# Kernel tuning notes

Hardware: AMD Instinct MI355X
Metric: run time of the kernel (lower is better)

Reference implementation:

```python
import jax, jax.numpy as jnp
import numpy as np

D = 128  # head dim

def setup_inputs() -> dict:
    key = jax.random.key(0)
    k1, k2, k3, k4, k5 = jax.random.split(key, 5)
    B, N, M, C1, C2 = 4, 4096, 4096, 1024, 1024
    x = jax.random.normal(k1, (B, N, C1), dtype=jnp.float32)
    y = jax.random.normal(k2, (B, M, C2), dtype=jnp.float32)
    # Linear(c, d, bias=False): out = inp @ W where W is [c, d]
    Wq = jax.random.normal(k3, (C1, D), dtype=jnp.float32) / np.sqrt(C1)
    Wk = jax.random.normal(k4, (C2, D), dtype=jnp.float32) / np.sqrt(C2)
    Wv = jax.random.normal(k5, (C2, D), dtype=jnp.float32) / np.sqrt(C2)
    return {"x": x, "y": y, "Wq": Wq, "Wk": Wk, "Wv": Wv}

def reference(x, y, Wq, Wk, Wv):
    q = x @ Wq                               # [B, N, d]
    k = y @ Wk                               # [B, M, d]
    v = y @ Wv                               # [B, M, d]
    scale = 1.0 / jnp.sqrt(jnp.asarray(D, dtype=q.dtype))
    a = jnp.einsum('bnd,bmd->bnm', q, k) * scale
    a = jax.nn.softmax(a, axis=-1)           # softmax FIRST
    a = jnp.triu(a, k=1)                     # post-softmax causal mask (keeps strict upper)
    out = jnp.einsum('bnm,bmd->bnd', a, v)   # [B, N, d]
    return out
```

## Files before the change

kernel.cpp:

```cpp
#include <hip/hip_runtime.h>
#include <hip/hip_bf16.h>
#include <stdint.h>


typedef __attribute__((ext_vector_type(8))) __bf16    bf16x8;
typedef __attribute__((ext_vector_type(4))) float     floatx4;
typedef __attribute__((ext_vector_type(8))) uint16_t  u16x8;
typedef __attribute__((ext_vector_type(4))) uint32_t  u32x4;

#define DEVFN __device__ __forceinline__

DEVFN uint16_t f32_to_bf16(float f) {
  uint32_t u = __builtin_bit_cast(uint32_t, f);
  u += 0x7FFFu + ((u >> 16) & 1u);
  return (uint16_t)(u >> 16);
}

DEVFN uint32_t bcast(float f) { return __builtin_bit_cast(uint32_t, f); }

DEVFN uint32_t pack2_bf16(float a, float b) {
  return ((bcast(a) + 0x8000u) >> 16) | ((bcast(b) + 0x8000u) & 0xFFFF0000u);
}

DEVFN u32x4 pack_bf16_8(float4 a0, float4 a1) {
  u32x4 o;
  o[0] = pack2_bf16(a0.x, a0.y);
  o[1] = pack2_bf16(a0.z, a0.w);
  o[2] = pack2_bf16(a1.x, a1.y);
  o[3] = pack2_bf16(a1.z, a1.w);
  return o;
}

DEVFN void gl2lds16(const void* g, void* l) {
  __builtin_amdgcn_global_load_lds(
      (const __attribute__((address_space(1))) void*)g,
      (__attribute__((address_space(3))) void*)l, 16, 0, 0);
}

__global__ __launch_bounds__(256) void wt_kernel(
    const float* __restrict__ Wq, const float* __restrict__ Wk,
    const float* __restrict__ Wv, uint16_t* __restrict__ wt) {
  int tid = blockIdx.x * 256 + threadIdx.x;
  int mat = tid >> 14;
  int rem = tid & 16383;
  int n  = rem & 127;
  int k0 = rem >> 7;
  const float* W = (mat == 0) ? Wq : ((mat == 1) ? Wk : Wv);
  u16x8 v;
#pragma unroll
  for (int j = 0; j < 8; ++j) v[j] = f32_to_bf16(W[(k0 * 8 + j) * 128 + n]);
  *(u16x8*)&wt[mat * (128 * 1024) + n * 1024 + k0 * 8] = v;
}

__global__ __launch_bounds__(512, 4) void qkv_kernel(
    const float* __restrict__ x, const float* __restrict__ y,
    const uint16_t* __restrict__ wt, uint16_t* __restrict__ q,
    uint16_t* __restrict__ k, uint16_t* __restrict__ vt) {
  constexpr int TB = 16384;
  __shared__ __align__(16) uint8_t sA[2 * TB];
  __shared__ __align__(16) uint8_t sW[2 * TB];
  const int t = threadIdx.x;
  const int mat = blockIdx.y, rt = blockIdx.x;
  const float* A = (mat == 0) ? x : y;
  const uint16_t* Wt = wt + mat * (128 * 1024);
  const int lane = t & 63, wv = t >> 6;
  const int wr = wv >> 1, wc = wv & 1;
  const int cidx = lane & 15, quad = lane >> 4;
  const int Arow0 = rt * 128;

  const int ar  = t >> 2;
  const int acq = t & 3;
  const float* aptr = &A[(size_t)(Arow0 + ar) * 1024 + acq * 16];
  const int aw0 = ar * 128 + (((2 * acq) ^ (ar & 7)) * 16);
  const int aw1 = ar * 128 + (((2 * acq + 1) ^ (ar & 7)) * 16);

  int wsrc[2], wdst[2];
#pragma unroll
  for (int i = 0; i < 2; ++i) {
    int G = i * 512 + t;
    int n = G >> 3, g = G & 7;
    wsrc[i] = n * 1024 + ((g ^ (n & 7)) * 8);
    wdst[i] = G * 16;
  }

  floatx4 acc[2][4];
#pragma unroll
  for (int rg = 0; rg < 2; ++rg)
#pragma unroll
    for (int ng = 0; ng < 4; ++ng) acc[rg][ng] = (floatx4){0.f, 0.f, 0.f, 0.f};

  float4 f4[4], g4[4];

#pragma unroll
  for (int i = 0; i < 2; ++i)
    gl2lds16(Wt + wsrc[i], sW + wdst[i]);
#pragma unroll
  for (int j = 0; j < 4; ++j) f4[j] = *(const float4*)(aptr + j * 4);

  for (int kt = 0; kt < 16; ++kt) {
    const int cur = kt & 1, nxt = cur ^ 1;
    if (kt < 15) {
      const int kc = (kt + 1) * 64;
#pragma unroll
      for (int i = 0; i < 2; ++i)
        gl2lds16(Wt + kc + wsrc[i], sW + nxt * TB + wdst[i]);
#pragma unroll
      for (int j = 0; j < 4; ++j) g4[j] = *(const float4*)(aptr + kc + j * 4);
      __builtin_amdgcn_sched_barrier(0);
      asm volatile("s_waitcnt vmcnt(6)" ::: "memory");
    } else {
      __builtin_amdgcn_sched_barrier(0);
      asm volatile("s_waitcnt vmcnt(0)" ::: "memory");
    }
    __builtin_amdgcn_sched_barrier(0);

    *(u32x4*)(sA + cur * TB + aw0) = pack_bf16_8(f4[0], f4[1]);
    *(u32x4*)(sA + cur * TB + aw1) = pack_bf16_8(f4[2], f4[3]);
    __builtin_amdgcn_sched_barrier(0);
    asm volatile("s_waitcnt lgkmcnt(0)" ::: "memory");
    __builtin_amdgcn_s_barrier();
    __builtin_amdgcn_sched_barrier(0);

    bf16x8 af[2][2];
#pragma unroll
    for (int rg = 0; rg < 2; ++rg)
#pragma unroll
      for (int ks = 0; ks < 2; ++ks)
        af[rg][ks] = *(const bf16x8*)
            (sA + cur * TB + (wr * 32 + rg * 16 + cidx) * 128 +
             (((ks * 4 + quad) ^ (cidx & 7)) * 16));
#pragma unroll
    for (int ng = 0; ng < 4; ++ng) {
      const int n = wc * 64 + ng * 16 + cidx;
      bf16x8 b0 = *(const bf16x8*)
          (sW + cur * TB + n * 128 + (((quad) ^ (cidx & 7)) * 16));
      bf16x8 b1 = *(const bf16x8*)
          (sW + cur * TB + n * 128 + (((4 + quad) ^ (cidx & 7)) * 16));
#pragma unroll
      for (int rg = 0; rg < 2; ++rg) {
        acc[rg][ng] = __builtin_amdgcn_mfma_f32_16x16x32_bf16(af[rg][0], b0, acc[rg][ng], 0, 0, 0);
        acc[rg][ng] = __builtin_amdgcn_mfma_f32_16x16x32_bf16(af[rg][1], b1, acc[rg][ng], 0, 0, 0);
      }
    }
    __builtin_amdgcn_sched_barrier(0);
    asm volatile("s_waitcnt lgkmcnt(0)" ::: "memory");
    __builtin_amdgcn_s_barrier();
    __builtin_amdgcn_sched_barrier(0);

    if (kt < 15) {
#pragma unroll
      for (int j = 0; j < 4; ++j) f4[j] = g4[j];
    }
  }

  if (mat < 2) {
    uint16_t* outp = (mat == 0) ? q : k;
#pragma unroll
    for (int rg = 0; rg < 2; ++rg)
#pragma unroll
      for (int r = 0; r < 4; ++r) {
        int row = Arow0 + wr * 32 + rg * 16 + quad * 4 + r;
#pragma unroll
        for (int ng = 0; ng < 4; ++ng)
          outp[row * 128 + wc * 64 + ng * 16 + cidx] = f32_to_bf16(acc[rg][ng][r]);
      }
  } else {
    int bq = rt >> 5;
    int mbase = (rt & 31) * 128;
#pragma unroll
    for (int rg = 0; rg < 2; ++rg)
#pragma unroll
      for (int r = 0; r < 4; ++r) {
        int m = mbase + wr * 32 + rg * 16 + quad * 4 + r;
#pragma unroll
        for (int ng = 0; ng < 4; ++ng)
          vt[(size_t)(bq * 128 + wc * 64 + ng * 16 + cidx) * 4096 + m] =
              f32_to_bf16(acc[rg][ng][r]);
      }
  }
}

__global__ __launch_bounds__(256, 2) void attn_kernel(
    const uint16_t* __restrict__ q, const uint16_t* __restrict__ k,
    const uint16_t* __restrict__ vt, float* __restrict__ opart,
    float* __restrict__ lpart, int mlen, int iters) {
  constexpr int KB = 16384, VB = 16384;
  __shared__ __align__(16) uint8_t sK[2 * KB];
  __shared__ __align__(16) uint8_t sV[2 * VB];
  const int t = threadIdx.x;
  const int lane = t & 63, wv = t >> 6;
  const int cidx = lane & 15, quad = lane >> 4;
  const int qt = blockIdx.x, h = blockIdx.y, b = blockIdx.z;
  const int qmin = qt * 128 + wv * 32;
  const int mbase = h * mlen;

  const uint16_t* qb = q + (size_t)(b * 4096) * 128;
  const uint8_t* kb = (const uint8_t*)(k + (size_t)(b * 4096) * 128);
  const uint8_t* vb = (const uint8_t*)(vt + (size_t)(b * 128) * 4096);

  const float SC = 0.12751744610657223f;

  int kOffL[4], vOffL[4], kLds[4], vLds[4];
#pragma unroll
  for (int u = 0; u < 4; ++u) {
    int r  = wv * 16 + u * 4 + (lane >> 4);
    int g  = (lane & 15) ^ (r & 15);
    kOffL[u] = r * 256 + g * 16;
    kLds[u]  = (wv * 16 + u * 4) * 256;
    int rv = wv * 32 + u * 8 + (lane >> 3);
    int gv = (lane & 7) ^ (rv & 7);
    vOffL[u] = rv * 8192 + gv * 16;
    vLds[u]  = (wv * 32 + u * 8) * 128;
  }

  bf16x8 qf[2][4];
#pragma unroll
  for (int qg = 0; qg < 2; ++qg)
#pragma unroll
    for (int ks = 0; ks < 4; ++ks)
      qf[qg][ks] = *(const bf16x8*)
          &qb[(qmin + qg * 16 + cidx) * 128 + ks * 32 + quad * 8];

  floatx4 O[2][8];
#pragma unroll
  for (int qg = 0; qg < 2; ++qg)
#pragma unroll
    for (int dg = 0; dg < 8; ++dg) O[qg][dg] = (floatx4){0.f, 0.f, 0.f, 0.f};
  float lsum[2] = {0.f, 0.f};

#pragma unroll
  for (int u = 0; u < 4; ++u) {
    gl2lds16(kb + (size_t)mbase * 256 + kOffL[u], sK + kLds[u]);
    gl2lds16(vb + (size_t)mbase * 2 + vOffL[u], sV + vLds[u]);
  }
  __syncthreads();

  for (int it = 0; it < iters; ++it) {
    const int m0 = mbase + it * 64;
    const int cur = it & 1, nxt = cur ^ 1;
    if (it + 1 < iters) {
      const int m1 = m0 + 64;
#pragma unroll
      for (int u = 0; u < 4; ++u) {
        gl2lds16(kb + (size_t)m1 * 256 + kOffL[u], sK + nxt * KB + kLds[u]);
        gl2lds16(vb + (size_t)m1 * 2 + vOffL[u], sV + nxt * VB + vLds[u]);
      }
    }

    floatx4 accST[2][4];
#pragma unroll
    for (int qg = 0; qg < 2; ++qg)
#pragma unroll
      for (int ng = 0; ng < 4; ++ng) accST[qg][ng] = (floatx4){0.f, 0.f, 0.f, 0.f};
#pragma unroll
    for (int ks = 0; ks < 4; ++ks)
#pragma unroll
      for (int ng = 0; ng < 4; ++ng) {
        bf16x8 kf = *(const bf16x8*)
            (sK + cur * KB + (ng * 16 + cidx) * 256 + ((ks * 4 + quad) ^ cidx) * 16);
        accST[0][ng] = __builtin_amdgcn_mfma_f32_16x16x32_bf16(kf, qf[0][ks], accST[0][ng], 0, 0, 0);
        accST[1][ng] = __builtin_amdgcn_mfma_f32_16x16x32_bf16(kf, qf[1][ks], accST[1][ng], 0, 0, 0);
      }

    float p[2][4][4];
#pragma unroll
    for (int qg = 0; qg < 2; ++qg)
#pragma unroll
      for (int ng = 0; ng < 4; ++ng)
#pragma unroll
        for (int r = 0; r < 4; ++r) {
          p[qg][ng][r] = exp2f(accST[qg][ng][r] * SC);
          lsum[qg] += p[qg][ng][r];
        }

    if (m0 + 63 > qmin) {
#pragma unroll
      for (int qg = 0; qg < 2; ++qg) {
        const int base = qmin + qg * 16;
        if (m0 < base + 16) {
#pragma unroll
          for (int ng = 0; ng < 4; ++ng)
#pragma unroll
            for (int r = 0; r < 4; ++r) {
              int m = m0 + ng * 16 + quad * 4 + r;
              int n = base + cidx;
              if (m <= n) p[qg][ng][r] = 0.f;
            }
        }
      }
      uint32_t pk[2][4][2];
#pragma unroll
      for (int qg = 0; qg < 2; ++qg)
#pragma unroll
        for (int ng = 0; ng < 4; ++ng) {
          pk[qg][ng][0] = pack2_bf16(p[qg][ng][0], p[qg][ng][1]);
          pk[qg][ng][1] = pack2_bf16(p[qg][ng][2], p[qg][ng][3]);
        }
#pragma unroll
      for (int ks = 0; ks < 2; ++ks) {
        bf16x8 pbv[2];
#pragma unroll
        for (int qg = 0; qg < 2; ++qg) {
          u32x4 pbw;
#pragma unroll
          for (int j2 = 0; j2 < 4; ++j2) {
            int lr = ((quad & 1) << 3) + 2 * j2;
            int srcl = ((lr >> 2) << 4) + cidx;
            uint32_t lo = (uint32_t)__shfl((int)pk[qg][2 * ks][j2 & 1], srcl);
            uint32_t hi = (uint32_t)__shfl((int)pk[qg][2 * ks + 1][j2 & 1], srcl);
            pbw[j2] = (quad & 2) ? hi : lo;
          }
          pbv[qg] = __builtin_bit_cast(bf16x8, pbw);
        }
#pragma unroll
        for (int dg = 0; dg < 8; ++dg) {
          bf16x8 vf = *(const bf16x8*)
              (sV + cur * VB + (dg * 16 + cidx) * 128 +
               (((ks * 4 + quad) ^ cidx) & 7) * 16);
          O[0][dg] = __builtin_amdgcn_mfma_f32_16x16x32_bf16(vf, pbv[0], O[0][dg], 0, 0, 0);
          O[1][dg] = __builtin_amdgcn_mfma_f32_16x16x32_bf16(vf, pbv[1], O[1][dg], 0, 0, 0);
        }
      }
    }
    __syncthreads();
  }

#pragma unroll
  for (int qg = 0; qg < 2; ++qg) {
    lsum[qg] += __shfl_xor(lsum[qg], 16);
    lsum[qg] += __shfl_xor(lsum[qg], 32);
    const int n = qmin + qg * 16 + cidx;
    float* op = opart + ((size_t)h * 16384 + b * 4096 + n) * 128;
#pragma unroll
    for (int dg = 0; dg < 8; ++dg)
      *(float4*)&op[dg * 16 + quad * 4] = __builtin_bit_cast(float4, O[qg][dg]);
    if (quad == 0) lpart[h * 16384 + b * 4096 + n] = lsum[qg];
  }
}

__global__ __launch_bounds__(256) void combine_kernel(
    const float* __restrict__ opart, const float* __restrict__ lpart,
    float* __restrict__ out, int hcount) {
  size_t i = (size_t)blockIdx.x * 256 + threadIdx.x;
  size_t e = i * 4;
  int row = (int)(e >> 7);
  float4 acc = {0.f, 0.f, 0.f, 0.f};
  float l = 0.f;
  for (int h = 0; h < hcount; ++h) {
    float4 ov = *(const float4*)&opart[(size_t)h * 2097152 + e];
    acc.x += ov.x; acc.y += ov.y; acc.z += ov.z; acc.w += ov.w;
    l += lpart[h * 16384 + row];
  }
  float inv = 1.0f / l;
  float4 o;
  o.x = acc.x * inv; o.y = acc.y * inv; o.z = acc.z * inv; o.w = acc.w * inv;
  *(float4*)&out[e] = o;
}

extern "C" void kernel_launch(void* const* d_in, const int* in_sizes, int n_in,
                              void* d_out, int out_size, void* d_ws, size_t ws_size,
                              hipStream_t stream) {
  const float* x  = (const float*)d_in[0];
  const float* y  = (const float*)d_in[1];
  const float* Wq = (const float*)d_in[2];
  const float* Wk = (const float*)d_in[3];
  const float* Wv = (const float*)d_in[4];
  uint16_t* ws = (uint16_t*)d_ws;
  uint16_t* wt = ws;
  uint16_t* q  = ws + 393216;
  uint16_t* k  = q + 2097152;
  uint16_t* vt = k + 2097152;
  float* opart = (float*)((char*)d_ws + 13369344);
  int hcount = (ws_size >= (size_t)13369344 + 4 * 8454144) ? 4 : 2;
  float* lpart = opart + (size_t)hcount * 2097152;
  float* o = (float*)d_out;
  int mlen = 4096 / hcount, iters = mlen / 64;

  hipLaunchKernelGGL(wt_kernel,      dim3(192),            dim3(256), 0, stream, Wq, Wk, Wv, wt);
  hipLaunchKernelGGL(qkv_kernel,     dim3(128, 3),         dim3(512), 0, stream, x, y, wt, q, k, vt);
  hipLaunchKernelGGL(attn_kernel,    dim3(32, hcount, 4),  dim3(256), 0, stream, q, k, vt, opart, lpart, mlen, iters);
  hipLaunchKernelGGL(combine_kernel, dim3(2048),           dim3(256), 0, stream, opart, lpart, o, hcount);
}
```

Measured before the change: 230.9 us.

## Interleave key split across heads, pair query tiles, read V from global

The attention kernel now splits keys across 4 partitions by stride (m mod 4) instead of contiguous ranges. Each block pairs a low and a mirrored high query tile to balance causal work. The V^T layout is permuted so each partition's keys are contiguous, and V fragments are loaded straight from global memory instead of staged in LDS. This frees LDS and allows 3 blocks per CU. s_setprio is added around the MFMA sections. The workspace-dependent hcount fallback is removed, so 4 partitions are always assumed, and the per-iteration V global loads may add latency.

```diff
diff --git a/kernel.cpp b/kernel.cpp
--- a/kernel.cpp
+++ b/kernel.cpp
@@ -129,6 +129,7 @@
         af[rg][ks] = *(const bf16x8*)
             (sA + cur * TB + (wr * 32 + rg * 16 + cidx) * 128 +
              (((ks * 4 + quad) ^ (cidx & 7)) * 16));
+    __builtin_amdgcn_s_setprio(1);
 #pragma unroll
     for (int ng = 0; ng < 4; ++ng) {
       const int n = wc * 64 + ng * 16 + cidx;
@@ -142,6 +143,7 @@
         acc[rg][ng] = __builtin_amdgcn_mfma_f32_16x16x32_bf16(af[rg][1], b1, acc[rg][ng], 0, 0, 0);
       }
     }
+    __builtin_amdgcn_s_setprio(0);
     __builtin_amdgcn_sched_barrier(0);
     asm volatile("s_waitcnt lgkmcnt(0)" ::: "memory");
     __builtin_amdgcn_s_barrier();
@@ -172,54 +174,50 @@
 #pragma unroll
       for (int r = 0; r < 4; ++r) {
         int m = mbase + wr * 32 + rg * 16 + quad * 4 + r;
+        int mp = ((m & 3) << 10) | (m >> 2);
 #pragma unroll
         for (int ng = 0; ng < 4; ++ng)
-          vt[(size_t)(bq * 128 + wc * 64 + ng * 16 + cidx) * 4096 + m] =
+          vt[(size_t)(bq * 128 + wc * 64 + ng * 16 + cidx) * 4096 + mp] =
               f32_to_bf16(acc[rg][ng][r]);
       }
   }
 }
 
-__global__ __launch_bounds__(256, 2) void attn_kernel(
+__global__ __launch_bounds__(256, 3) void attn_kernel(
     const uint16_t* __restrict__ q, const uint16_t* __restrict__ k,
     const uint16_t* __restrict__ vt, float* __restrict__ opart,
-    float* __restrict__ lpart, int mlen, int iters) {
-  constexpr int KB = 16384, VB = 16384;
+    float* __restrict__ lpart) {
+  constexpr int KB = 16384;
   __shared__ __align__(16) uint8_t sK[2 * KB];
-  __shared__ __align__(16) uint8_t sV[2 * VB];
   const int t = threadIdx.x;
   const int lane = t & 63, wv = t >> 6;
   const int cidx = lane & 15, quad = lane >> 4;
-  const int qt = blockIdx.x, h = blockIdx.y, b = blockIdx.z;
-  const int qmin = qt * 128 + wv * 32;
-  const int mbase = h * mlen;
+  const int qtp = blockIdx.x, h = blockIdx.y, b = blockIdx.z;
+  const int qbase0 = qtp * 64 + wv * 16;
+  const int qbase1 = 4032 - qtp * 64 + wv * 16;
 
   const uint16_t* qb = q + (size_t)(b * 4096) * 128;
-  const uint8_t* kb = (const uint8_t*)(k + (size_t)(b * 4096) * 128);
+  const uint8_t* kb = (const uint8_t*)(k + (size_t)(b * 4096) * 128) + h * 256;
   const uint8_t* vb = (const uint8_t*)(vt + (size_t)(b * 128) * 4096);
 
   const float SC = 0.12751744610657223f;
 
-  int kOffL[4], vOffL[4], kLds[4], vLds[4];
+  int kOffL[4], kLds[4];
 #pragma unroll
   for (int u = 0; u < 4; ++u) {
     int r  = wv * 16 + u * 4 + (lane >> 4);
     int g  = (lane & 15) ^ (r & 15);
-    kOffL[u] = r * 256 + g * 16;
+    kOffL[u] = r * 1024 + g * 16;
     kLds[u]  = (wv * 16 + u * 4) * 256;
-    int rv = wv * 32 + u * 8 + (lane >> 3);
-    int gv = (lane & 7) ^ (rv & 7);
-    vOffL[u] = rv * 8192 + gv * 16;
-    vLds[u]  = (wv * 32 + u * 8) * 128;
-  }
-
+  }
+
+  const int qn[2] = {qbase0 + cidx, qbase1 + cidx};
   bf16x8 qf[2][4];
 #pragma unroll
   for (int qg = 0; qg < 2; ++qg)
 #pragma unroll
     for (int ks = 0; ks < 4; ++ks)
-      qf[qg][ks] = *(const bf16x8*)
-          &qb[(qmin + qg * 16 + cidx) * 128 + ks * 32 + quad * 8];
+      qf[qg][ks] = *(const bf16x8*)&qb[qn[qg] * 128 + ks * 32 + quad * 8];
 
   floatx4 O[2][8];
 #pragma unroll
@@ -229,22 +227,17 @@
   float lsum[2] = {0.f, 0.f};
 
 #pragma unroll
-  for (int u = 0; u < 4; ++u) {
-    gl2lds16(kb + (size_t)mbase * 256 + kOffL[u], sK + kLds[u]);
-    gl2lds16(vb + (size_t)mbase * 2 + vOffL[u], sV + vLds[u]);
-  }
+  for (int u = 0; u < 4; ++u)
+    gl2lds16(kb + kOffL[u], sK + kLds[u]);
   __syncthreads();
 
-  for (int it = 0; it < iters; ++it) {
-    const int m0 = mbase + it * 64;
+  for (int it = 0; it < 16; ++it) {
     const int cur = it & 1, nxt = cur ^ 1;
-    if (it + 1 < iters) {
-      const int m1 = m0 + 64;
-#pragma unroll
-      for (int u = 0; u < 4; ++u) {
-        gl2lds16(kb + (size_t)m1 * 256 + kOffL[u], sK + nxt * KB + kLds[u]);
-        gl2lds16(vb + (size_t)m1 * 2 + vOffL[u], sV + nxt * VB + vLds[u]);
-      }
+    if (it < 15) {
+#pragma unroll
+      for (int u = 0; u < 4; ++u)
+        gl2lds16(kb + (size_t)((it + 1) * 64) * 1024 + kOffL[u],
+                 sK + nxt * KB + kLds[u]);
     }
 
     floatx4 accST[2][4];
@@ -252,6 +245,7 @@
     for (int qg = 0; qg < 2; ++qg)
 #pragma unroll
       for (int ng = 0; ng < 4; ++ng) accST[qg][ng] = (floatx4){0.f, 0.f, 0.f, 0.f};
+    __builtin_amdgcn_s_setprio(1);
 #pragma unroll
     for (int ks = 0; ks < 4; ++ks)
 #pragma unroll
@@ -261,6 +255,7 @@
         accST[0][ng] = __builtin_amdgcn_mfma_f32_16x16x32_bf16(kf, qf[0][ks], accST[0][ng], 0, 0, 0);
         accST[1][ng] = __builtin_amdgcn_mfma_f32_16x16x32_bf16(kf, qf[1][ks], accST[1][ng], 0, 0, 0);
       }
+    __builtin_amdgcn_s_setprio(0);
 
     float p[2][4][4];
 #pragma unroll
@@ -273,52 +268,53 @@
           lsum[qg] += p[qg][ng][r];
         }
 
-    if (m0 + 63 > qmin) {
+    const int mgmin = h + 4 * (it * 64);
+    const int mgmax = mgmin + 4 * 63;
+    const bool act0 = mgmax > qbase0;
+    const bool act1 = mgmax > qbase1;
+    if (act0 | act1) {
 #pragma unroll
       for (int qg = 0; qg < 2; ++qg) {
-        const int base = qmin + qg * 16;
-        if (m0 < base + 16) {
+        const bool act = qg ? act1 : act0;
+        if (!act) continue;
+        const int qbs = qg ? qbase1 : qbase0;
+        if (mgmin <= qbs + 15) {
 #pragma unroll
           for (int ng = 0; ng < 4; ++ng)
 #pragma unroll
             for (int r = 0; r < 4; ++r) {
-              int m = m0 + ng * 16 + quad * 4 + r;
-              int n = base + cidx;
+              int m = h + 4 * (it * 64 + ng * 16 + quad * 4 + r);
+              int n = qbs + cidx;
               if (m <= n) p[qg][ng][r] = 0.f;
             }
         }
-      }
-      uint32_t pk[2][4][2];
-#pragma unroll
-      for (int qg = 0; qg < 2; ++qg)
+        uint32_t pk[4][2];
 #pragma unroll
         for (int ng = 0; ng < 4; ++ng) {
-          pk[qg][ng][0] = pack2_bf16(p[qg][ng][0], p[qg][ng][1]);
-          pk[qg][ng][1] = pack2_bf16(p[qg][ng][2], p[qg][ng][3]);
+          pk[ng][0] = pack2_bf16(p[qg][ng][0], p[qg][ng][1]);
+          pk[ng][1] = pack2_bf16(p[qg][ng][2], p[qg][ng][3]);
         }
 #pragma unroll
-      for (int ks = 0; ks < 2; ++ks) {
-        bf16x8 pbv[2];
-#pragma unroll
-        for (int qg = 0; qg < 2; ++qg) {
+        for (int ks = 0; ks < 2; ++ks) {
           u32x4 pbw;
 #pragma unroll
           for (int j2 = 0; j2 < 4; ++j2) {
             int lr = ((quad & 1) << 3) + 2 * j2;
             int srcl = ((lr >> 2) << 4) + cidx;
-            uint32_t lo = (uint32_t)__shfl((int)pk[qg][2 * ks][j2 & 1], srcl);
-            uint32_t hi = (uint32_t)__shfl((int)pk[qg][2 * ks + 1][j2 & 1], srcl);
+            uint32_t lo = (uint32_t)__shfl((int)pk[2 * ks][j2 & 1], srcl);
+            uint32_t hi = (uint32_t)__shfl((int)pk[2 * ks + 1][j2 & 1], srcl);
             pbw[j2] = (quad & 2) ? hi : lo;
           }
-          pbv[qg] = __builtin_bit_cast(bf16x8, pbw);
-        }
-#pragma unroll
-        for (int dg = 0; dg < 8; ++dg) {
-          bf16x8 vf = *(const bf16x8*)
-              (sV + cur * VB + (dg * 16 + cidx) * 128 +
-               (((ks * 4 + quad) ^ cidx) & 7) * 16);
-          O[0][dg] = __builtin_amdgcn_mfma_f32_16x16x32_bf16(vf, pbv[0], O[0][dg], 0, 0, 0);
-          O[1][dg] = __builtin_amdgcn_mfma_f32_16x16x32_bf16(vf, pbv[1], O[1][dg], 0, 0, 0);
+          bf16x8 pbv = __builtin_bit_cast(bf16x8, pbw);
+          __builtin_amdgcn_s_setprio(1);
+#pragma unroll
+          for (int dg = 0; dg < 8; ++dg) {
+            bf16x8 vf = *(const bf16x8*)
+                (vb + (size_t)(dg * 16 + cidx) * 8192 +
+                 (size_t)(h * 1024 + it * 64) * 2 + (ks * 4 + quad) * 16);
+            O[qg][dg] = __builtin_amdgcn_mfma_f32_16x16x32_bf16(vf, pbv, O[qg][dg], 0, 0, 0);
+          }
+          __builtin_amdgcn_s_setprio(0);
         }
       }
     }
@@ -329,7 +325,7 @@
   for (int qg = 0; qg < 2; ++qg) {
     lsum[qg] += __shfl_xor(lsum[qg], 16);
     lsum[qg] += __shfl_xor(lsum[qg], 32);
-    const int n = qmin + qg * 16 + cidx;
+    const int n = qn[qg];
     float* op = opart + ((size_t)h * 16384 + b * 4096 + n) * 128;
 #pragma unroll
     for (int dg = 0; dg < 8; ++dg)
@@ -371,13 +367,11 @@
   uint16_t* k  = q + 2097152;
   uint16_t* vt = k + 2097152;
   float* opart = (float*)((char*)d_ws + 13369344);
-  int hcount = (ws_size >= (size_t)13369344 + 4 * 8454144) ? 4 : 2;
-  float* lpart = opart + (size_t)hcount * 2097152;
+  float* lpart = opart + (size_t)4 * 2097152;
   float* o = (float*)d_out;
-  int mlen = 4096 / hcount, iters = mlen / 64;
-
-  hipLaunchKernelGGL(wt_kernel,      dim3(192),            dim3(256), 0, stream, Wq, Wk, Wv, wt);
-  hipLaunchKernelGGL(qkv_kernel,     dim3(128, 3),         dim3(512), 0, stream, x, y, wt, q, k, vt);
-  hipLaunchKernelGGL(attn_kernel,    dim3(32, hcount, 4),  dim3(256), 0, stream, q, k, vt, opart, lpart, mlen, iters);
-  hipLaunchKernelGGL(combine_kernel, dim3(2048),           dim3(256), 0, stream, opart, lpart, o, hcount);
-}
+
+  hipLaunchKernelGGL(wt_kernel,      dim3(192),        dim3(256), 0, stream, Wq, Wk, Wv, wt);
+  hipLaunchKernelGGL(qkv_kernel,     dim3(128, 3),     dim3(512), 0, stream, x, y, wt, q, k, vt);
+  hipLaunchKernelGGL(attn_kernel,    dim3(32, 4, 4),   dim3(256), 0, stream, q, k, vt, opart, lpart);
+  hipLaunchKernelGGL(combine_kernel, dim3(2048),       dim3(256), 0, stream, opart, lpart, o, 4);
+}
```

Result: slower. 316.6 us (+37.1%).

## Fuse split-KV combine into attention via last-block ticket and raise MFMA priority

Applied to the files above, without the earlier changes.

Removes the separate combine kernel. Each attention block now increments a per-(batch, query-tile) atomic counter after writing its partials, and the last block to arrive reduces the partial outputs and row sums and writes the normalized result. The counters are zeroed inside qkv_kernel. The change also wraps both MFMA loops in s_setprio(1)/s_setprio(0) to favor matrix-issuing waves. This saves one kernel launch and its scheduling gap, at the cost of threadfence and atomic overhead and a tail where a few blocks do the reduction serially.

```diff
diff --git a/kernel.cpp b/kernel.cpp
--- a/kernel.cpp
+++ b/kernel.cpp
@@ -55,12 +55,14 @@
 __global__ __launch_bounds__(512, 4) void qkv_kernel(
     const float* __restrict__ x, const float* __restrict__ y,
     const uint16_t* __restrict__ wt, uint16_t* __restrict__ q,
-    uint16_t* __restrict__ k, uint16_t* __restrict__ vt) {
+    uint16_t* __restrict__ k, uint16_t* __restrict__ vt,
+    int* __restrict__ cnt) {
   constexpr int TB = 16384;
   __shared__ __align__(16) uint8_t sA[2 * TB];
   __shared__ __align__(16) uint8_t sW[2 * TB];
   const int t = threadIdx.x;
   const int mat = blockIdx.y, rt = blockIdx.x;
+  if (mat == 0 && rt == 0 && t < 128) cnt[t] = 0;
   const float* A = (mat == 0) ? x : y;
   const uint16_t* Wt = wt + mat * (128 * 1024);
   const int lane = t & 63, wv = t >> 6;
@@ -183,10 +185,12 @@
 __global__ __launch_bounds__(256, 2) void attn_kernel(
     const uint16_t* __restrict__ q, const uint16_t* __restrict__ k,
     const uint16_t* __restrict__ vt, float* __restrict__ opart,
-    float* __restrict__ lpart, int mlen, int iters) {
+    float* __restrict__ lpart, float* __restrict__ out,
+    int* __restrict__ cnt, int mlen, int iters, int hcount) {
   constexpr int KB = 16384, VB = 16384;
   __shared__ __align__(16) uint8_t sK[2 * KB];
   __shared__ __align__(16) uint8_t sV[2 * VB];
+  __shared__ int ticket_s;
   const int t = threadIdx.x;
   const int lane = t & 63, wv = t >> 6;
   const int cidx = lane & 15, quad = lane >> 4;
@@ -252,6 +256,7 @@
     for (int qg = 0; qg < 2; ++qg)
 #pragma unroll
       for (int ng = 0; ng < 4; ++ng) accST[qg][ng] = (floatx4){0.f, 0.f, 0.f, 0.f};
+    __builtin_amdgcn_s_setprio(1);
 #pragma unroll
     for (int ks = 0; ks < 4; ++ks)
 #pragma unroll
@@ -261,6 +266,7 @@
         accST[0][ng] = __builtin_amdgcn_mfma_f32_16x16x32_bf16(kf, qf[0][ks], accST[0][ng], 0, 0, 0);
         accST[1][ng] = __builtin_amdgcn_mfma_f32_16x16x32_bf16(kf, qf[1][ks], accST[1][ng], 0, 0, 0);
       }
+    __builtin_amdgcn_s_setprio(0);
 
     float p[2][4][4];
 #pragma unroll
@@ -312,6 +318,7 @@
           }
           pbv[qg] = __builtin_bit_cast(bf16x8, pbw);
         }
+        __builtin_amdgcn_s_setprio(1);
 #pragma unroll
         for (int dg = 0; dg < 8; ++dg) {
           bf16x8 vf = *(const bf16x8*)
@@ -320,6 +327,7 @@
           O[0][dg] = __builtin_amdgcn_mfma_f32_16x16x32_bf16(vf, pbv[0], O[0][dg], 0, 0, 0);
           O[1][dg] = __builtin_amdgcn_mfma_f32_16x16x32_bf16(vf, pbv[1], O[1][dg], 0, 0, 0);
         }
+        __builtin_amdgcn_s_setprio(0);
       }
     }
     __syncthreads();
@@ -336,25 +344,32 @@
       *(float4*)&op[dg * 16 + quad * 4] = __builtin_bit_cast(float4, O[qg][dg]);
     if (quad == 0) lpart[h * 16384 + b * 4096 + n] = lsum[qg];
   }
-}
-
-__global__ __launch_bounds__(256) void combine_kernel(
-    const float* __restrict__ opart, const float* __restrict__ lpart,
-    float* __restrict__ out, int hcount) {
-  size_t i = (size_t)blockIdx.x * 256 + threadIdx.x;
-  size_t e = i * 4;
-  int row = (int)(e >> 7);
-  float4 acc = {0.f, 0.f, 0.f, 0.f};
-  float l = 0.f;
-  for (int h = 0; h < hcount; ++h) {
-    float4 ov = *(const float4*)&opart[(size_t)h * 2097152 + e];
-    acc.x += ov.x; acc.y += ov.y; acc.z += ov.z; acc.w += ov.w;
-    l += lpart[h * 16384 + row];
-  }
-  float inv = 1.0f / l;
-  float4 o;
-  o.x = acc.x * inv; o.y = acc.y * inv; o.z = acc.z * inv; o.w = acc.w * inv;
-  *(float4*)&out[e] = o;
+
+  __threadfence();
+  if (t == 0) ticket_s = atomicAdd(&cnt[b * 32 + qt], 1);
+  __syncthreads();
+  if (ticket_s == hcount - 1) {
+    __threadfence();
+    const float4* op4 = (const float4*)opart;
+    float4* out4 = (float4*)out;
+    const int b4 = b * 131072 + qt * 4096;
+    for (int i = 0; i < 16; ++i) {
+      int j2 = b4 + t + i * 256;
+      int rowg = j2 >> 5;
+      float4 acc = {0.f, 0.f, 0.f, 0.f};
+      float l = 0.f;
+      for (int h2 = 0; h2 < hcount; ++h2) {
+        float4 ov = op4[(size_t)h2 * 524288 + j2];
+        acc.x += ov.x; acc.y += ov.y; acc.z += ov.z; acc.w += ov.w;
+        l += lpart[h2 * 16384 + rowg];
+      }
+      float inv = 1.0f / l;
+      float4 o4;
+      o4.x = acc.x * inv; o4.y = acc.y * inv;
+      o4.z = acc.z * inv; o4.w = acc.w * inv;
+      out4[j2] = o4;
+    }
+  }
 }
 
 extern "C" void kernel_launch(void* const* d_in, const int* in_sizes, int n_in,
@@ -371,13 +386,13 @@
   uint16_t* k  = q + 2097152;
   uint16_t* vt = k + 2097152;
   float* opart = (float*)((char*)d_ws + 13369344);
-  int hcount = (ws_size >= (size_t)13369344 + 4 * 8454144) ? 4 : 2;
+  int hcount = (ws_size >= (size_t)13369344 + 4 * 8454144 + 512) ? 4 : 2;
   float* lpart = opart + (size_t)hcount * 2097152;
+  int* cnt = (int*)((char*)d_ws + 13369344 + (size_t)hcount * 8454144);
   float* o = (float*)d_out;
   int mlen = 4096 / hcount, iters = mlen / 64;
 
-  hipLaunchKernelGGL(wt_kernel,      dim3(192),            dim3(256), 0, stream, Wq, Wk, Wv, wt);
-  hipLaunchKernelGGL(qkv_kernel,     dim3(128, 3),         dim3(512), 0, stream, x, y, wt, q, k, vt);
-  hipLaunchKernelGGL(attn_kernel,    dim3(32, hcount, 4),  dim3(256), 0, stream, q, k, vt, opart, lpart, mlen, iters);
-  hipLaunchKernelGGL(combine_kernel, dim3(2048),           dim3(256), 0, stream, opart, lpart, o, hcount);
-}
+  hipLaunchKernelGGL(wt_kernel,   dim3(192),           dim3(256), 0, stream, Wq, Wk, Wv, wt);
+  hipLaunchKernelGGL(qkv_kernel,  dim3(128, 3),        dim3(512), 0, stream, x, y, wt, q, k, vt, cnt);
+  hipLaunchKernelGGL(attn_kernel, dim3(32, hcount, 4), dim3(256), 0, stream, q, k, vt, opart, lpart, o, cnt, mlen, iters, hcount);
+}
```

Result: slower. 319.4 us (+38.3%).

## Single-buffer K tile, split K/V prefetch with fine-grained waits, raise occupancy to 3

Applied to the files above, without the earlier changes.

Drops the K shared buffer from double to single so LDS per block shrinks, and raises the launch bound to 3 blocks per CU. V is still double-buffered and prefetched at the top of each iteration. The next K tile is loaded after the QK^T MFMAs, behind an extra barrier. Explicit vmcnt/lgkmcnt waits and s_barrier with sched_barrier replace __syncthreads, and setprio raises wave priority around the MFMA loops. The aim is better latency hiding through occupancy, at the cost of an extra barrier per iteration, less K prefetch distance, and register pressure under the tighter bound.

```diff
diff --git a/kernel.cpp b/kernel.cpp
--- a/kernel.cpp
+++ b/kernel.cpp
@@ -180,12 +180,12 @@
   }
 }
 
-__global__ __launch_bounds__(256, 2) void attn_kernel(
+__global__ __launch_bounds__(256, 3) void attn_kernel(
     const uint16_t* __restrict__ q, const uint16_t* __restrict__ k,
     const uint16_t* __restrict__ vt, float* __restrict__ opart,
     float* __restrict__ lpart, int mlen, int iters) {
   constexpr int KB = 16384, VB = 16384;
-  __shared__ __align__(16) uint8_t sK[2 * KB];
+  __shared__ __align__(16) uint8_t sK[KB];
   __shared__ __align__(16) uint8_t sV[2 * VB];
   const int t = threadIdx.x;
   const int lane = t & 63, wv = t >> 6;
@@ -229,38 +229,58 @@
   float lsum[2] = {0.f, 0.f};
 
 #pragma unroll
-  for (int u = 0; u < 4; ++u) {
+  for (int u = 0; u < 4; ++u)
     gl2lds16(kb + (size_t)mbase * 256 + kOffL[u], sK + kLds[u]);
+#pragma unroll
+  for (int u = 0; u < 4; ++u)
     gl2lds16(vb + (size_t)mbase * 2 + vOffL[u], sV + vLds[u]);
-  }
-  __syncthreads();
-
+
+  int cur = 0;
   for (int it = 0; it < iters; ++it) {
     const int m0 = mbase + it * 64;
-    const int cur = it & 1, nxt = cur ^ 1;
     if (it + 1 < iters) {
       const int m1 = m0 + 64;
 #pragma unroll
-      for (int u = 0; u < 4; ++u) {
-        gl2lds16(kb + (size_t)m1 * 256 + kOffL[u], sK + nxt * KB + kLds[u]);
-        gl2lds16(vb + (size_t)m1 * 2 + vOffL[u], sV + nxt * VB + vLds[u]);
-      }
-    }
+      for (int u = 0; u < 4; ++u)
+        gl2lds16(vb + (size_t)m1 * 2 + vOffL[u], sV + (cur ^ 1) * VB + vLds[u]);
+      __builtin_amdgcn_sched_barrier(0);
+      asm volatile("s_waitcnt vmcnt(4)" ::: "memory");
+    } else {
+      __builtin_amdgcn_sched_barrier(0);
+      asm volatile("s_waitcnt vmcnt(0)" ::: "memory");
+    }
+    __builtin_amdgcn_sched_barrier(0);
+    __builtin_amdgcn_s_barrier();
+    __builtin_amdgcn_sched_barrier(0);
 
     floatx4 accST[2][4];
 #pragma unroll
     for (int qg = 0; qg < 2; ++qg)
 #pragma unroll
       for (int ng = 0; ng < 4; ++ng) accST[qg][ng] = (floatx4){0.f, 0.f, 0.f, 0.f};
+    __builtin_amdgcn_s_setprio(1);
 #pragma unroll
     for (int ks = 0; ks < 4; ++ks)
 #pragma unroll
       for (int ng = 0; ng < 4; ++ng) {
         bf16x8 kf = *(const bf16x8*)
-            (sK + cur * KB + (ng * 16 + cidx) * 256 + ((ks * 4 + quad) ^ cidx) * 16);
+            (sK + (ng * 16 + cidx) * 256 + ((ks * 4 + quad) ^ cidx) * 16);
         accST[0][ng] = __builtin_amdgcn_mfma_f32_16x16x32_bf16(kf, qf[0][ks], accST[0][ng], 0, 0, 0);
         accST[1][ng] = __builtin_amdgcn_mfma_f32_16x16x32_bf16(kf, qf[1][ks], accST[1][ng], 0, 0, 0);
       }
+    __builtin_amdgcn_s_setprio(0);
+    __builtin_amdgcn_sched_barrier(0);
+    asm volatile("s_waitcnt lgkmcnt(0)" ::: "memory");
+    __builtin_amdgcn_s_barrier();
+    __builtin_amdgcn_sched_barrier(0);
+
+    if (it + 1 < iters) {
+      const int m1 = m0 + 64;
+#pragma unroll
+      for (int u = 0; u < 4; ++u)
+        gl2lds16(kb + (size_t)m1 * 256 + kOffL[u], sK + kLds[u]);
+    }
+    __builtin_amdgcn_sched_barrier(0);
 
     float p[2][4][4];
 #pragma unroll
@@ -312,6 +332,7 @@
           }
           pbv[qg] = __builtin_bit_cast(bf16x8, pbw);
         }
+        __builtin_amdgcn_s_setprio(1);
 #pragma unroll
         for (int dg = 0; dg < 8; ++dg) {
           bf16x8 vf = *(const bf16x8*)
@@ -320,9 +341,14 @@
           O[0][dg] = __builtin_amdgcn_mfma_f32_16x16x32_bf16(vf, pbv[0], O[0][dg], 0, 0, 0);
           O[1][dg] = __builtin_amdgcn_mfma_f32_16x16x32_bf16(vf, pbv[1], O[1][dg], 0, 0, 0);
         }
-      }
-    }
-    __syncthreads();
+        __builtin_amdgcn_s_setprio(0);
+      }
+    }
+    __builtin_amdgcn_sched_barrier(0);
+    asm volatile("s_waitcnt lgkmcnt(0)" ::: "memory");
+    __builtin_amdgcn_s_barrier();
+    __builtin_amdgcn_sched_barrier(0);
+    cur ^= 1;
   }
 
 #pragma unroll
```

New measurement: 336.9 us. +45.9%, slower.
